# Optimization experiments

Measured on AMD Instinct MI355X. Metric: run time of the kernel, lower is better.

Reference implementation:

```python
import jax, jax.numpy as jnp
import numpy as np

B = 64            # number of graphs
NODES_PER_G = 64  # real nodes per graph
N_MAX = 128       # max_num_nodes (dense padding)
NT = B * NODES_PER_G   # 4096 total nodes
E = 65536         # edges (and pairs)
H = 64            # hidden_dim
D_NODE = 32
POLY = 16


def setup_inputs() -> dict:
    key = jax.random.key(0)
    ks = jax.random.split(key, 12)
    node_x = jax.random.normal(ks[0], (NT, D_NODE), dtype=jnp.float32)
    loop_x = jax.random.normal(ks[1], (NT, POLY), dtype=jnp.float32)
    edge_attr = jax.random.normal(ks[2], (E, D_NODE), dtype=jnp.float32)
    pair_x = jax.random.normal(ks[3], (E, POLY), dtype=jnp.float32)
    W_node = jax.random.normal(ks[4], (D_NODE, H), dtype=jnp.float32) / np.sqrt(D_NODE)
    W_loop = jax.random.normal(ks[5], (POLY, H), dtype=jnp.float32) / np.sqrt(POLY)
    W_edge = jax.random.normal(ks[6], (D_NODE, H), dtype=jnp.float32) / np.sqrt(D_NODE)
    W_pair = jax.random.normal(ks[7], (POLY, H), dtype=jnp.float32) / np.sqrt(POLY)
    # sorted graph assignment: 64 nodes per graph
    batch = (jnp.arange(NT, dtype=jnp.int32) // NODES_PER_G).astype(jnp.int32)
    # intra-graph edges: global index = graph*NODES_PER_G + local
    epg = E // B  # edges per graph
    eg = (jnp.arange(E, dtype=jnp.int32) // epg)
    e_loc = jax.random.randint(ks[8], (2, E), 0, NODES_PER_G, dtype=jnp.int32)
    edge_index = eg[None, :] * NODES_PER_G + e_loc
    p_loc = jax.random.randint(ks[9], (2, E), 0, NODES_PER_G, dtype=jnp.int32)
    pair_index = eg[None, :] * NODES_PER_G + p_loc
    return {
        "node_x": node_x, "loop_x": loop_x, "edge_attr": edge_attr, "pair_x": pair_x,
        "W_node": W_node, "W_loop": W_loop, "W_edge": W_edge, "W_pair": W_pair,
        "batch": batch, "edge_index": edge_index, "pair_index": pair_index,
    }


def _positions(batch):
    # position of each node within its graph (to_dense_batch semantics)
    counts = jax.ops.segment_sum(jnp.ones_like(batch), batch, num_segments=B)
    starts = jnp.concatenate([jnp.zeros((1,), counts.dtype), jnp.cumsum(counts)[:-1]])
    return jnp.arange(batch.shape[0], dtype=batch.dtype) - starts[batch].astype(batch.dtype)


def _to_dense_adj(index, batch, pos, h):
    b = batch[index[0]]
    r = pos[index[0]]
    c = pos[index[1]]
    dense = jnp.zeros((B, N_MAX, N_MAX, H), dtype=h.dtype)
    return dense.at[b, r, c].add(h)  # duplicates are summed, as in to_dense_adj


def reference(node_x, loop_x, edge_attr, pair_x, W_node, W_loop, W_edge, W_pair,
              batch, edge_index, pair_index):
    pos = _positions(batch)
    # node + loop encoders (linear), then scatter to dense batch [B, N, H]
    node_h = node_x @ W_node + loop_x @ W_loop
    dense_node_h = jnp.zeros((B, N_MAX, H), dtype=node_h.dtype).at[batch, pos].set(node_h)
    dense_node_mask = jnp.zeros((B, N_MAX), dtype=bool).at[batch, pos].set(True)
    # permute (0,2,1) -> [B, H, N], then diag_embed -> [B, H, N, N]
    dnh = jnp.transpose(dense_node_h, (0, 2, 1))
    ar = jnp.arange(N_MAX)
    dense_diag_h = jnp.zeros((B, H, N_MAX, N_MAX), dtype=dnh.dtype).at[:, :, ar, ar].set(dnh)
    # edge + pair encoders, scatter to dense adjacency [B, N, N, H]
    edge_h = edge_attr @ W_edge
    pair_h = pair_x @ W_pair
    dense_pair = _to_dense_adj(edge_index, batch, pos, edge_h) \
               + _to_dense_adj(pair_index, batch, pos, pair_h)
    # permute (0,3,1,2) -> [B, H, N, N], add diagonal node features
    dense_pair_h = jnp.transpose(dense_pair, (0, 3, 1, 2)) + dense_diag_h
    return dense_pair_h, dense_node_mask
```

## Files before the change

kernel.cpp:

```cpp
#include <hip/hip_runtime.h>

#define NTOT  4096
#define NG    64
#define NMAXD 128
#define HD    64
#define NEDGE 65536
#define EPG   (NEDGE / NG)
#define NPG   (NTOT / NG)

typedef float f4 __attribute__((ext_vector_type(4)));

__device__ __forceinline__ int lowb(const int* __restrict__ batch, int key) {
  int lo = 0, hi = NTOT;
  while (lo < hi) { const int mid = (lo + hi) >> 1;
    if (batch[mid] < key) lo = mid + 1; else hi = mid; }
  return lo;
}

__global__ __launch_bounds__(256) void prep_all_kernel(
    const int* __restrict__ eI, const int* __restrict__ pI,
    const int* __restrict__ batch,
    int* __restrict__ rcE, int* __restrict__ rcP, int* __restrict__ rcN,
    int* __restrict__ counts) {
  const int i = blockIdx.x * 256 + threadIdx.x;
  if (i < NEDGE) {
    const int n0 = eI[i], n1 = eI[NEDGE + i];
    const int b0 = batch[n0], b1 = batch[n1];
    rcE[i] = (b0 << 16) | ((n0 - lowb(batch, b0)) << 8) | (n1 - lowb(batch, b1));
  } else if (i < 2 * NEDGE) {
    const int j = i - NEDGE;
    const int n0 = pI[j], n1 = pI[NEDGE + j];
    const int b0 = batch[n0], b1 = batch[n1];
    rcP[j] = (b0 << 16) | ((n0 - lowb(batch, b0)) << 8) | (n1 - lowb(batch, b1));
  } else if (i < 2 * NEDGE + NTOT) {
    const int j = i - 2 * NEDGE;
    const int b = batch[j];
    const int p = j - lowb(batch, b);
    rcN[j] = (b << 16) | (p << 8) | p;
  } else if (i < 2 * NEDGE + NTOT + NG) {
    const int g = i - 2 * NEDGE - NTOT;
    counts[g] = lowb(batch, g + 1) - lowb(batch, g);
  }
}

#define HQ 4
#define SCT 512
__global__ __launch_bounds__(SCT) void fused_scatter_kernel(
    const float* __restrict__ node_x, const float* __restrict__ loop_x,
    const float* __restrict__ edge_attr, const float* __restrict__ pair_x,
    const float* __restrict__ Wn, const float* __restrict__ Wl,
    const float* __restrict__ We, const float* __restrict__ Wp,
    const int* __restrict__ rcE, const int* __restrict__ rcP,
    const int* __restrict__ rcN, const int* __restrict__ counts,
    float* __restrict__ out, float* __restrict__ mask) {
  __shared__ float acc[HQ * 4096];
  __shared__ f4 WcE[32];
  __shared__ f4 WcP[16];
  __shared__ f4 WcN[48];

  const int tid = threadIdx.x;
  const int d  = (int)blockIdx.x;
  const int g  = ((d & 7) << 3) | ((d >> 3) & 7);
  const int h0 = (d >> 6) * HQ;

  if (tid < 32)       WcE[tid]            = *(const f4*)&We[tid * HD + h0];
  else if (tid < 48)  WcP[tid - 32]       = *(const f4*)&Wp[(tid - 32) * HD + h0];
  else if (tid < 80)  WcN[tid - 48]       = *(const f4*)&Wn[(tid - 48) * HD + h0];
  else if (tid < 96)  WcN[32 + tid - 80]  = *(const f4*)&Wl[(tid - 80) * HD + h0];
  for (int i = tid; i < HQ * 1024; i += SCT) ((f4*)acc)[i] = (f4)(0.f);
  __syncthreads();

  const int wid = tid >> 6;
  if (wid >= 4) {
    const int tz = tid - 256;
#pragma unroll
    for (int t = 0; t < HQ; ++t) {
      f4* plane = (f4*)(out + ((size_t)g * HD + h0 + t) * NMAXD * NMAXD);
#pragma unroll
      for (int k = 0; k < 4; ++k) {
        const int idx = tz + k * 256;
        plane[(idx >> 4) * 32 + 16 + (idx & 15)] = (f4)(0.f);
      }
#pragma unroll
      for (int k = 0; k < 8; ++k)
        plane[2048 + tz + k * 256] = (f4)(0.f);
    }
    if (h0 == 0) {
      const int cg = counts[g];
      for (int i = tz; i < NMAXD; i += 256)
        mask[(size_t)g * NMAXD + i] = (i < cg) ? 1.0f : 0.0f;
    }
  } else {
#pragma unroll
    for (int k = 0; k < 4; ++k) {
      const int j = g * EPG + tid + k * 256;
      const f4* xr = (const f4*)(edge_attr + (size_t)j * 32);
      f4 d4 = (f4)(0.f);
#pragma unroll
      for (int k4 = 0; k4 < 8; ++k4) {
        const f4 x = xr[k4];
#pragma unroll
        for (int u = 0; u < 4; ++u) d4 += x[u] * WcE[k4 * 4 + u];
      }
      const int code = rcE[j];
      const int b = code >> 16, r = (code >> 8) & 255, c = code & 255;
      if (b == g && r < 64 && c < 64) {
        const int a = r * 64 + c;
        unsafeAtomicAdd(&acc[a], d4.x);          unsafeAtomicAdd(&acc[4096 + a], d4.y);
        unsafeAtomicAdd(&acc[8192 + a], d4.z);   unsafeAtomicAdd(&acc[12288 + a], d4.w);
      } else {
        unsafeAtomicAdd(&out[(((size_t)b * HD + h0 + 0) * NMAXD + r) * NMAXD + c], d4.x);
        unsafeAtomicAdd(&out[(((size_t)b * HD + h0 + 1) * NMAXD + r) * NMAXD + c], d4.y);
        unsafeAtomicAdd(&out[(((size_t)b * HD + h0 + 2) * NMAXD + r) * NMAXD + c], d4.z);
        unsafeAtomicAdd(&out[(((size_t)b * HD + h0 + 3) * NMAXD + r) * NMAXD + c], d4.w);
      }
    }

#pragma unroll
    for (int k = 0; k < 4; ++k) {
      const int j = g * EPG + tid + k * 256;
      const f4* xr = (const f4*)(pair_x + (size_t)j * 16);
      f4 d4 = (f4)(0.f);
#pragma unroll
      for (int k4 = 0; k4 < 4; ++k4) {
        const f4 x = xr[k4];
#pragma unroll
        for (int u = 0; u < 4; ++u) d4 += x[u] * WcP[k4 * 4 + u];
      }
      const int code = rcP[j];
      const int b = code >> 16, r = (code >> 8) & 255, c = code & 255;
      if (b == g && r < 64 && c < 64) {
        const int a = r * 64 + c;
        unsafeAtomicAdd(&acc[a], d4.x);          unsafeAtomicAdd(&acc[4096 + a], d4.y);
        unsafeAtomicAdd(&acc[8192 + a], d4.z);   unsafeAtomicAdd(&acc[12288 + a], d4.w);
      } else {
        unsafeAtomicAdd(&out[(((size_t)b * HD + h0 + 0) * NMAXD + r) * NMAXD + c], d4.x);
        unsafeAtomicAdd(&out[(((size_t)b * HD + h0 + 1) * NMAXD + r) * NMAXD + c], d4.y);
        unsafeAtomicAdd(&out[(((size_t)b * HD + h0 + 2) * NMAXD + r) * NMAXD + c], d4.z);
        unsafeAtomicAdd(&out[(((size_t)b * HD + h0 + 3) * NMAXD + r) * NMAXD + c], d4.w);
      }
    }

    if (tid < NPG) {
      const int j = g * NPG + tid;
      const f4* xr = (const f4*)(node_x + (size_t)j * 32);
      const f4* lr = (const f4*)(loop_x + (size_t)j * 16);
      f4 d4 = (f4)(0.f);
#pragma unroll
      for (int k4 = 0; k4 < 8; ++k4) {
        const f4 x = xr[k4];
#pragma unroll
        for (int u = 0; u < 4; ++u) d4 += x[u] * WcN[k4 * 4 + u];
      }
#pragma unroll
      for (int k4 = 0; k4 < 4; ++k4) {
        const f4 x = lr[k4];
#pragma unroll
        for (int u = 0; u < 4; ++u) d4 += x[u] * WcN[32 + k4 * 4 + u];
      }
      const int code = rcN[j];
      const int b = code >> 16, r = (code >> 8) & 255, c = code & 255;
      if (b == g && r < 64 && c < 64) {
        const int a = r * 64 + c;
        unsafeAtomicAdd(&acc[a], d4.x);          unsafeAtomicAdd(&acc[4096 + a], d4.y);
        unsafeAtomicAdd(&acc[8192 + a], d4.z);   unsafeAtomicAdd(&acc[12288 + a], d4.w);
      } else {
        unsafeAtomicAdd(&out[(((size_t)b * HD + h0 + 0) * NMAXD + r) * NMAXD + c], d4.x);
        unsafeAtomicAdd(&out[(((size_t)b * HD + h0 + 1) * NMAXD + r) * NMAXD + c], d4.y);
        unsafeAtomicAdd(&out[(((size_t)b * HD + h0 + 2) * NMAXD + r) * NMAXD + c], d4.z);
        unsafeAtomicAdd(&out[(((size_t)b * HD + h0 + 3) * NMAXD + r) * NMAXD + c], d4.w);
      }
    }
  }
  __syncthreads();

#pragma unroll
  for (int t = 0; t < HQ; ++t) {
    f4* plane = (f4*)(out + ((size_t)g * HD + h0 + t) * NMAXD * NMAXD);
#pragma unroll
    for (int k = 0; k < 2; ++k) {
      const int idx = tid + k * SCT;
      const int r = idx >> 4, c4 = idx & 15;
      plane[r * 32 + c4] = *(const f4*)&acc[t * 4096 + r * 64 + c4 * 4];
    }
  }
}

extern "C" void kernel_launch(void* const* d_in, const int* in_sizes, int n_in,
                              void* d_out, int out_size, void* d_ws, size_t ws_size,
                              hipStream_t stream) {
  const float* node_x    = (const float*)d_in[0];
  const float* loop_x    = (const float*)d_in[1];
  const float* edge_attr = (const float*)d_in[2];
  const float* pair_x    = (const float*)d_in[3];
  const float* W_node    = (const float*)d_in[4];
  const float* W_loop    = (const float*)d_in[5];
  const float* W_edge    = (const float*)d_in[6];
  const float* W_pair    = (const float*)d_in[7];
  const int*   batch     = (const int*)d_in[8];
  const int*   edge_index = (const int*)d_in[9];
  const int*   pair_index = (const int*)d_in[10];

  float* out  = (float*)d_out;
  float* mask = out + (size_t)NG * HD * NMAXD * NMAXD;

  int* rcE    = (int*)d_ws;
  int* rcP    = rcE + NEDGE;
  int* rcN    = rcP + NEDGE;
  int* counts = rcN + NTOT;

  const int prep_items = 2 * NEDGE + NTOT + NG;
  prep_all_kernel<<<(prep_items + 255) / 256, 256, 0, stream>>>(
      edge_index, pair_index, batch, rcE, rcP, rcN, counts);
  fused_scatter_kernel<<<NG * 16, SCT, 0, stream>>>(node_x, loop_x, edge_attr,
      pair_x, W_node, W_loop, W_edge, W_pair, rcE, rcP, rcN, counts, out, mask);
}
```

Measured before the change: 73.39 us.

## Transpose input features to column-major f4 planes in prep kernel for coalesced loads

The prep kernel now also copies edge_attr, pair_x, node_x and loop_x into workspace buffers, laid out as f4 planes ordered by feature chunk and then row. In the scatter kernel, adjacent threads then read adjacent f4 values instead of strided 128B/64B rows. This aims to improve coalescing of the feature reads, which are repeated across the 16 h-quarter blocks per graph. The cost is an extra full read and write of about 12.6 MB of inputs in the prep kernel, plus more workspace use.

```diff
diff --git a/kernel.cpp b/kernel.cpp
--- a/kernel.cpp
+++ b/kernel.cpp
@@ -17,28 +17,41 @@
   return lo;
 }
 
+#define PREP_GRID 3793
 __global__ __launch_bounds__(256) void prep_all_kernel(
+    const float* __restrict__ node_x, const float* __restrict__ loop_x,
+    const float* __restrict__ edge_attr, const float* __restrict__ pair_x,
     const int* __restrict__ eI, const int* __restrict__ pI,
     const int* __restrict__ batch,
+    f4* __restrict__ edT, f4* __restrict__ pT,
+    f4* __restrict__ nT, f4* __restrict__ lT,
     int* __restrict__ rcE, int* __restrict__ rcP, int* __restrict__ rcN,
     int* __restrict__ counts) {
-  const int i = blockIdx.x * 256 + threadIdx.x;
-  if (i < NEDGE) {
-    const int n0 = eI[i], n1 = eI[NEDGE + i];
+  int t = blockIdx.x * 256 + threadIdx.x;
+  if (t < 8 * NEDGE) { edT[(t & 7) * NEDGE + (t >> 3)] = ((const f4*)edge_attr)[t]; return; }
+  t -= 8 * NEDGE;
+  if (t < 4 * NEDGE) { pT[(t & 3) * NEDGE + (t >> 2)] = ((const f4*)pair_x)[t]; return; }
+  t -= 4 * NEDGE;
+  if (t < 8 * NTOT)  { nT[(t & 7) * NTOT + (t >> 3)] = ((const f4*)node_x)[t]; return; }
+  t -= 8 * NTOT;
+  if (t < 4 * NTOT)  { lT[(t & 3) * NTOT + (t >> 2)] = ((const f4*)loop_x)[t]; return; }
+  t -= 4 * NTOT;
+  if (t < NEDGE) {
+    const int n0 = eI[t], n1 = eI[NEDGE + t];
     const int b0 = batch[n0], b1 = batch[n1];
-    rcE[i] = (b0 << 16) | ((n0 - lowb(batch, b0)) << 8) | (n1 - lowb(batch, b1));
-  } else if (i < 2 * NEDGE) {
-    const int j = i - NEDGE;
+    rcE[t] = (b0 << 16) | ((n0 - lowb(batch, b0)) << 8) | (n1 - lowb(batch, b1));
+  } else if (t < 2 * NEDGE) {
+    const int j = t - NEDGE;
     const int n0 = pI[j], n1 = pI[NEDGE + j];
     const int b0 = batch[n0], b1 = batch[n1];
     rcP[j] = (b0 << 16) | ((n0 - lowb(batch, b0)) << 8) | (n1 - lowb(batch, b1));
-  } else if (i < 2 * NEDGE + NTOT) {
-    const int j = i - 2 * NEDGE;
+  } else if (t < 2 * NEDGE + NTOT) {
+    const int j = t - 2 * NEDGE;
     const int b = batch[j];
     const int p = j - lowb(batch, b);
     rcN[j] = (b << 16) | (p << 8) | p;
-  } else if (i < 2 * NEDGE + NTOT + NG) {
-    const int g = i - 2 * NEDGE - NTOT;
+  } else if (t < 2 * NEDGE + NTOT + NG) {
+    const int g = t - 2 * NEDGE - NTOT;
     counts[g] = lowb(batch, g + 1) - lowb(batch, g);
   }
 }
@@ -46,8 +59,8 @@
 #define HQ 4
 #define SCT 512
 __global__ __launch_bounds__(SCT) void fused_scatter_kernel(
-    const float* __restrict__ node_x, const float* __restrict__ loop_x,
-    const float* __restrict__ edge_attr, const float* __restrict__ pair_x,
+    const f4* __restrict__ edT, const f4* __restrict__ pT,
+    const f4* __restrict__ nT, const f4* __restrict__ lT,
     const float* __restrict__ Wn, const float* __restrict__ Wl,
     const float* __restrict__ We, const float* __restrict__ Wp,
     const int* __restrict__ rcE, const int* __restrict__ rcP,
@@ -91,16 +104,17 @@
         mask[(size_t)g * NMAXD + i] = (i < cg) ? 1.0f : 0.0f;
     }
   } else {
+    const int la = tid;
+
 #pragma unroll
     for (int k = 0; k < 4; ++k) {
-      const int j = g * EPG + tid + k * 256;
-      const f4* xr = (const f4*)(edge_attr + (size_t)j * 32);
+      const int j = g * EPG + la + k * 256;
       f4 d4 = (f4)(0.f);
 #pragma unroll
       for (int k4 = 0; k4 < 8; ++k4) {
-        const f4 x = xr[k4];
-#pragma unroll
-        for (int u = 0; u < 4; ++u) d4 += x[u] * WcE[k4 * 4 + u];
+        const f4 x = edT[(size_t)k4 * NEDGE + j];
+        d4 += x.x * WcE[k4 * 4 + 0] + x.y * WcE[k4 * 4 + 1]
+            + x.z * WcE[k4 * 4 + 2] + x.w * WcE[k4 * 4 + 3];
       }
       const int code = rcE[j];
       const int b = code >> 16, r = (code >> 8) & 255, c = code & 255;
@@ -118,14 +132,13 @@
 
 #pragma unroll
     for (int k = 0; k < 4; ++k) {
-      const int j = g * EPG + tid + k * 256;
-      const f4* xr = (const f4*)(pair_x + (size_t)j * 16);
+      const int j = g * EPG + la + k * 256;
       f4 d4 = (f4)(0.f);
 #pragma unroll
       for (int k4 = 0; k4 < 4; ++k4) {
-        const f4 x = xr[k4];
-#pragma unroll
-        for (int u = 0; u < 4; ++u) d4 += x[u] * WcP[k4 * 4 + u];
+        const f4 x = pT[(size_t)k4 * NEDGE + j];
+        d4 += x.x * WcP[k4 * 4 + 0] + x.y * WcP[k4 * 4 + 1]
+            + x.z * WcP[k4 * 4 + 2] + x.w * WcP[k4 * 4 + 3];
       }
       const int code = rcP[j];
       const int b = code >> 16, r = (code >> 8) & 255, c = code & 255;
@@ -141,22 +154,20 @@
       }
     }
 
-    if (tid < NPG) {
-      const int j = g * NPG + tid;
-      const f4* xr = (const f4*)(node_x + (size_t)j * 32);
-      const f4* lr = (const f4*)(loop_x + (size_t)j * 16);
+    if (la < NPG) {
+      const int j = g * NPG + la;
       f4 d4 = (f4)(0.f);
 #pragma unroll
       for (int k4 = 0; k4 < 8; ++k4) {
-        const f4 x = xr[k4];
-#pragma unroll
-        for (int u = 0; u < 4; ++u) d4 += x[u] * WcN[k4 * 4 + u];
+        const f4 x = nT[(size_t)k4 * NTOT + j];
+        d4 += x.x * WcN[k4 * 4 + 0] + x.y * WcN[k4 * 4 + 1]
+            + x.z * WcN[k4 * 4 + 2] + x.w * WcN[k4 * 4 + 3];
       }
 #pragma unroll
       for (int k4 = 0; k4 < 4; ++k4) {
-        const f4 x = lr[k4];
-#pragma unroll
-        for (int u = 0; u < 4; ++u) d4 += x[u] * WcN[32 + k4 * 4 + u];
+        const f4 x = lT[(size_t)k4 * NTOT + j];
+        d4 += x.x * WcN[32 + k4 * 4 + 0] + x.y * WcN[32 + k4 * 4 + 1]
+            + x.z * WcN[32 + k4 * 4 + 2] + x.w * WcN[32 + k4 * 4 + 3];
       }
       const int code = rcN[j];
       const int b = code >> 16, r = (code >> 8) & 255, c = code & 255;
@@ -208,10 +219,14 @@
   int* rcP    = rcE + NEDGE;
   int* rcN    = rcP + NEDGE;
   int* counts = rcN + NTOT;
-
-  const int prep_items = 2 * NEDGE + NTOT + NG;
-  prep_all_kernel<<<(prep_items + 255) / 256, 256, 0, stream>>>(
-      edge_index, pair_index, batch, rcE, rcP, rcN, counts);
-  fused_scatter_kernel<<<NG * 16, SCT, 0, stream>>>(node_x, loop_x, edge_attr,
-      pair_x, W_node, W_loop, W_edge, W_pair, rcE, rcP, rcN, counts, out, mask);
-}
+  f4*  edT    = (f4*)(counts + NG);
+  f4*  pT     = edT + (size_t)8 * NEDGE;
+  f4*  nT     = pT + (size_t)4 * NEDGE;
+  f4*  lT     = nT + (size_t)8 * NTOT;
+
+  prep_all_kernel<<<PREP_GRID, 256, 0, stream>>>(node_x, loop_x, edge_attr,
+      pair_x, edge_index, pair_index, batch, edT, pT, nT, lT,
+      rcE, rcP, rcN, counts);
+  fused_scatter_kernel<<<NG * 16, SCT, 0, stream>>>(edT, pT, nT, lT,
+      W_node, W_loop, W_edge, W_pair, rcE, rcP, rcN, counts, out, mask);
+}
```

Measured after the change: 96.74 us. 31.8% more time.
